# Performance work log

Measured on AMD Instinct MI355X. Metric: run time of the kernel, lower is better.

The kernel has to match this reference:

```python
import jax, jax.numpy as jnp
import numpy as np

N_NODES = 100000
N_EDGES = 1250000
D = 64


def _sage_conv(x, src, dst, W_l, b_l, W_r, n_nodes):
    # message = x[src]; scatter-mean onto dst; then lin_l(mean) + lin_r(x)
    msg = x[src]                                               # [E, D]
    agg = jax.ops.segment_sum(msg, dst, num_segments=n_nodes)  # [N, D]
    cnt = jax.ops.segment_sum(jnp.ones((src.shape[0],), x.dtype), dst,
                              num_segments=n_nodes)            # [N]
    mean = agg / jnp.maximum(cnt, 1.0)[:, None]
    return mean @ W_l + b_l + x @ W_r


def setup_inputs() -> dict:
    key = jax.random.key(0)
    ks = jax.random.split(key, 8)
    s = 1.0 / np.sqrt(D)
    x = jax.random.normal(ks[0], (N_NODES, D), dtype=jnp.float32)
    edge_index = jax.random.randint(ks[1], (2, N_EDGES), 0, N_NODES, dtype=jnp.int32)
    W_l1 = jax.random.normal(ks[2], (D, D), dtype=jnp.float32) * s
    b_l1 = jnp.zeros((D,), jnp.float32)
    W_r1 = jax.random.normal(ks[3], (D, D), dtype=jnp.float32) * s
    W_l2 = jax.random.normal(ks[4], (D, D), dtype=jnp.float32) * s
    b_l2 = jnp.zeros((D,), jnp.float32)
    W_r2 = jax.random.normal(ks[5], (D, D), dtype=jnp.float32) * s
    return {"x": x, "edge_index": edge_index,
            "W_l1": W_l1, "b_l1": b_l1, "W_r1": W_r1,
            "W_l2": W_l2, "b_l2": b_l2, "W_r2": W_r2}


def reference(x, edge_index, W_l1, b_l1, W_r1, W_l2, b_l2, W_r2):
    src, dst = edge_index[0], edge_index[1]
    n = x.shape[0]
    h = jax.nn.relu(_sage_conv(x, src, dst, W_l1, b_l1, W_r1, n))
    return _sage_conv(h, src, dst, W_l2, b_l2, W_r2, n)
```

## Files before the change

### kernel.cpp

```cpp
#include <hip/hip_runtime.h>

#define N_NODES 100000
#define N_EDGES 1250000
#define D 64

#define BIN_SHIFT 9
#define BIN_NODES 512
#define NBINS ((N_NODES + BIN_NODES - 1) >> BIN_SHIFT)
#define BIN_CAP 7168
#define SLAB 8704
#define CHUNK 4096
#define ZERO_NODE N_NODES

typedef __attribute__((ext_vector_type(8))) short short8;
typedef __attribute__((ext_vector_type(4))) float f32x4;

__device__ inline unsigned short f2bf(float f) {
    unsigned int u = __float_as_uint(f);
    unsigned int r = (u + 0x7fffu + ((u >> 16) & 1u)) >> 16;
    return (unsigned short)r;
}
__device__ inline float4 unpack_bf4(uint2 u) {
    float4 f;
    f.x = __uint_as_float(u.x << 16);
    f.y = __uint_as_float(u.x & 0xffff0000u);
    f.z = __uint_as_float(u.y << 16);
    f.w = __uint_as_float(u.y & 0xffff0000u);
    return f;
}

__global__ __launch_bounds__(256)
void convert_zero_kernel(const float4* __restrict__ xin, ushort4* __restrict__ xb,
                         int n4, int* __restrict__ bin_cnt,
                         unsigned int* __restrict__ xb_zrow,
                         unsigned int* __restrict__ h_zrow,
                         const float* __restrict__ Wl1, const float* __restrict__ Wr1,
                         const float* __restrict__ Wl2, const float* __restrict__ Wr2,
                         unsigned short* __restrict__ wt) {
    int i = blockIdx.x * 256 + threadIdx.x;
    if (i < n4) {
        float4 v = xin[i];
        ushort4 u;
        u.x = f2bf(v.x); u.y = f2bf(v.y); u.z = f2bf(v.z); u.w = f2bf(v.w);
        xb[i] = u;
    }
    if (i < NBINS) bin_cnt[i] = 0;
    if (i < 32) { xb_zrow[i] = 0u; h_zrow[i] = 0u; }
    if (i < 2 * 64 * 128) {
        int layer = i >> 13;
        int n = (i >> 7) & 63;
        int k = i & 127;
        const float* W = layer ? (k < 64 ? Wl2 : Wr2) : (k < 64 ? Wl1 : Wr1);
        float v = W[(k & 63) * D + n];
        wt[i] = f2bf(v);
    }
}

__global__ __launch_bounds__(256)
void bin_kernel(const int* __restrict__ src, const int* __restrict__ dst,
                int* __restrict__ bin_cnt, int* __restrict__ slabs) {
    __shared__ int lhist[NBINS];
    __shared__ int lstart[NBINS];
    __shared__ int lbase[NBINS];
    __shared__ int lcur[NBINS];
    __shared__ int pscan[256];
    __shared__ int sval[CHUNK];
    __shared__ int sdst[CHUNK];

    const int t = threadIdx.x;
    const int e0 = blockIdx.x * CHUNK;
    int cnt = N_EDGES - e0; if (cnt > CHUNK) cnt = CHUNK;

    for (int i = t; i < NBINS; i += 256) lhist[i] = 0;
    __syncthreads();

    for (int i = t; i < cnt; i += 256)
        atomicAdd(&lhist[dst[e0 + i] >> BIN_SHIFT], 1);
    __syncthreads();

    int h = (t < NBINS) ? lhist[t] : 0;
    pscan[t] = h;
    __syncthreads();
    for (int off = 1; off < 256; off <<= 1) {
        int x = (t >= off) ? pscan[t - off] : 0;
        __syncthreads();
        pscan[t] += x;
        __syncthreads();
    }
    if (t < NBINS) {
        int excl = pscan[t] - h;
        lstart[t] = excl;
        lcur[t] = excl;
        lbase[t] = (h > 0) ? atomicAdd(&bin_cnt[t], h) : 0;
    }
    __syncthreads();

    for (int i = t; i < cnt; i += 256) {
        int d = dst[e0 + i];
        int s = src[e0 + i];
        int b = d >> BIN_SHIFT;
        int slot = atomicAdd(&lcur[b], 1);
        int rank = slot - lstart[b];
        sval[slot] = (s << BIN_SHIFT) | (d & (BIN_NODES - 1));
        int gp = lbase[b] + rank;
        sdst[slot] = (gp < BIN_CAP) ? (b * SLAB + gp) : -1;
    }
    __syncthreads();

    for (int i = t; i < cnt; i += 256) {
        int dd = sdst[i];
        if (dd >= 0) slabs[dd] = sval[i];
    }
}

__global__ __launch_bounds__(256)
void bin_sort_kernel(int* __restrict__ slabs, const int* __restrict__ bin_cnt,
                     int* __restrict__ deg_out, int* __restrict__ rstart_out) {
    __shared__ int hist[BIN_NODES];
    __shared__ int cur[BIN_NODES];
    __shared__ int pscan[256];
    __shared__ int stage[BIN_CAP];

    const int b = blockIdx.x;
    const int t = threadIdx.x;
    int cnt = bin_cnt[b]; if (cnt > BIN_CAP) cnt = BIN_CAP;
    const int nb0 = b << BIN_SHIFT;
    const int nn = (N_NODES - nb0 < BIN_NODES) ? (N_NODES - nb0) : BIN_NODES;
    const int slab0 = b * SLAB;

    hist[t] = 0; hist[t + 256] = 0;
    __syncthreads();

    for (int i = t; i < cnt; i += 256) {
        int p = slabs[slab0 + i];
        stage[i] = p;
        atomicAdd(&hist[p & (BIN_NODES - 1)], 1);
    }
    __syncthreads();

    int h0 = hist[2 * t], h1 = hist[2 * t + 1];
    int ph0 = (h0 + 3) & ~3, ph1 = (h1 + 3) & ~3;
    int pv = ph0 + ph1;
    pscan[t] = pv;
    __syncthreads();
    for (int off = 1; off < 256; off <<= 1) {
        int x = (t >= off) ? pscan[t - off] : 0;
        __syncthreads();
        pscan[t] += x;
        __syncthreads();
    }
    int pairExcl = pscan[t] - pv;
    int s0 = pairExcl, s1 = pairExcl + ph0;
    cur[2 * t] = s0;
    cur[2 * t + 1] = s1;
    if (2 * t < nn) {
        deg_out[nb0 + 2 * t] = h0;
        rstart_out[nb0 + 2 * t] = slab0 + s0;
        for (int i = h0; i < ph0; ++i) slabs[slab0 + s0 + i] = ZERO_NODE;
    }
    if (2 * t + 1 < nn) {
        deg_out[nb0 + 2 * t + 1] = h1;
        rstart_out[nb0 + 2 * t + 1] = slab0 + s1;
        for (int i = h1; i < ph1; ++i) slabs[slab0 + s1 + i] = ZERO_NODE;
    }
    __syncthreads();

    for (int i = t; i < cnt; i += 256) {
        int p = stage[i];
        int pos = atomicAdd(&cur[p & (BIN_NODES - 1)], 1);
        slabs[slab0 + pos] = p >> BIN_SHIFT;
    }
}

template <typename TOUT>
__global__ __launch_bounds__(256, 8)
void fused_layer_kernel(const unsigned short* __restrict__ xin,
                        const int* __restrict__ rstart,
                        const int* __restrict__ deg,
                        const int* __restrict__ sorted_src,
                        const unsigned short* __restrict__ wt,
                        const float* __restrict__ bl,
                        TOUT* __restrict__ out,
                        int relu) {
    __shared__ __align__(16) unsigned short sA[32][136];

    const uint2* __restrict__ xin64 = (const uint2*)xin;

    const int tid = threadIdx.x;
    const int row0 = blockIdx.x * 32;

    const int wave = tid >> 6;
    const int lane = tid & 63;
    const int q  = lane >> 4;
    const int f2 = lane & 15;

    for (int r = wave; r < 32; r += 4) {
        int n = row0 + r;
        float4 a = make_float4(0.f, 0.f, 0.f, 0.f);
        int dg = deg[n];
        int pdg = (dg + 3) & ~3;
        int st = rstart[n];
        uint2 xraw = xin64[(size_t)n * 16 + f2];

        for (int base = 0; base < pdg; base += 64) {
            int m = pdg - base; if (m > 64) m = 64;
            int idx = 0;
            if (lane < m) idx = sorted_src[st + base + lane];
            int quads = m >> 2;
            float4 c0 = make_float4(0.f, 0.f, 0.f, 0.f);
            float4 c1 = make_float4(0.f, 0.f, 0.f, 0.f);
            float4 c2 = make_float4(0.f, 0.f, 0.f, 0.f);
            float4 c3 = make_float4(0.f, 0.f, 0.f, 0.f);
            int t = 0;
            for (; t + 4 <= quads; t += 4) {
                int sA_ = __shfl(idx, 4 * t + q);
                int sB_ = __shfl(idx, 4 * t + 4 + q);
                int sC_ = __shfl(idx, 4 * t + 8 + q);
                int sD_ = __shfl(idx, 4 * t + 12 + q);
                float4 fA = unpack_bf4(xin64[(size_t)sA_ * 16 + f2]);
                float4 fB = unpack_bf4(xin64[(size_t)sB_ * 16 + f2]);
                float4 fC = unpack_bf4(xin64[(size_t)sC_ * 16 + f2]);
                float4 fD = unpack_bf4(xin64[(size_t)sD_ * 16 + f2]);
                c0.x += fA.x; c0.y += fA.y; c0.z += fA.z; c0.w += fA.w;
                c1.x += fB.x; c1.y += fB.y; c1.z += fB.z; c1.w += fB.w;
                c2.x += fC.x; c2.y += fC.y; c2.z += fC.z; c2.w += fC.w;
                c3.x += fD.x; c3.y += fD.y; c3.z += fD.z; c3.w += fD.w;
            }
            for (; t + 2 <= quads; t += 2) {
                int sA_ = __shfl(idx, 4 * t + q);
                int sB_ = __shfl(idx, 4 * t + 4 + q);
                float4 fA = unpack_bf4(xin64[(size_t)sA_ * 16 + f2]);
                float4 fB = unpack_bf4(xin64[(size_t)sB_ * 16 + f2]);
                c0.x += fA.x; c0.y += fA.y; c0.z += fA.z; c0.w += fA.w;
                c1.x += fB.x; c1.y += fB.y; c1.z += fB.z; c1.w += fB.w;
            }
            for (; t < quads; ++t) {
                int sA_ = __shfl(idx, 4 * t + q);
                float4 fA = unpack_bf4(xin64[(size_t)sA_ * 16 + f2]);
                c0.x += fA.x; c0.y += fA.y; c0.z += fA.z; c0.w += fA.w;
            }
            a.x += (c0.x + c1.x) + (c2.x + c3.x);
            a.y += (c0.y + c1.y) + (c2.y + c3.y);
            a.z += (c0.z + c1.z) + (c2.z + c3.z);
            a.w += (c0.w + c1.w) + (c2.w + c3.w);
        }

        a.x += __shfl_xor(a.x, 16); a.y += __shfl_xor(a.y, 16);
        a.z += __shfl_xor(a.z, 16); a.w += __shfl_xor(a.w, 16);
        a.x += __shfl_xor(a.x, 32); a.y += __shfl_xor(a.y, 32);
        a.z += __shfl_xor(a.z, 32); a.w += __shfl_xor(a.w, 32);

        float inv = 1.0f / (float)(dg > 0 ? dg : 1);
        if (q == 0) {
            unsigned int p0 = (unsigned int)f2bf(a.x * inv) |
                              ((unsigned int)f2bf(a.y * inv) << 16);
            unsigned int p1 = (unsigned int)f2bf(a.z * inv) |
                              ((unsigned int)f2bf(a.w * inv) << 16);
            *(uint2*)&sA[r][f2 * 4] = make_uint2(p0, p1);
            *(uint2*)&sA[r][64 + f2 * 4] = xraw;
        }
    }
    __syncthreads();

    const int tm = wave & 1;
    const int tn0 = (wave >> 1) * 2;
    const int mrow = tm * 16 + (lane & 15);
    const int kq = (lane >> 4) * 8;

    short8 afr[4];
#pragma unroll
    for (int kk = 0; kk < 4; ++kk)
        afr[kk] = *(const short8*)&sA[mrow][kk * 32 + kq];

#pragma unroll
    for (int ti = 0; ti < 2; ++ti) {
        const int tn = tn0 + ti;
        const int col = tn * 16 + (lane & 15);
        float bias = bl[col];
        f32x4 acc = {bias, bias, bias, bias};
#pragma unroll
        for (int kk = 0; kk < 4; ++kk) {
            short8 bfr = *(const short8*)&wt[col * 128 + kk * 32 + kq];
            acc = __builtin_amdgcn_mfma_f32_16x16x32_bf16(afr[kk], bfr, acc, 0, 0, 0);
        }
        const int r0 = row0 + tm * 16 + (lane >> 4) * 4;
#pragma unroll
        for (int reg = 0; reg < 4; ++reg) {
            float o = relu ? fmaxf(acc[reg], 0.f) : acc[reg];
            if constexpr (__hip_internal::is_same<TOUT, unsigned short>::value)
                out[(size_t)(r0 + reg) * D + col] = f2bf(o);
            else
                out[(size_t)(r0 + reg) * D + col] = o;
        }
    }
}

extern "C" void kernel_launch(void* const* d_in, const int* in_sizes, int n_in,
                              void* d_out, int out_size, void* d_ws, size_t ws_size,
                              hipStream_t stream) {
    const float* x   = (const float*)d_in[0];
    const int*   ei  = (const int*)d_in[1];
    const float* Wl1 = (const float*)d_in[2];
    const float* b1  = (const float*)d_in[3];
    const float* Wr1 = (const float*)d_in[4];
    const float* Wl2 = (const float*)d_in[5];
    const float* b2  = (const float*)d_in[6];
    const float* Wr2 = (const float*)d_in[7];

    const int* src = ei;
    const int* dst = ei + N_EDGES;

    int* slabs   = (int*)d_ws;
    int* bin_cnt = slabs + (size_t)NBINS * SLAB;
    int* deg     = bin_cnt + 256;
    int* rstart  = deg + N_NODES;
    unsigned short* wt_all = (unsigned short*)(rstart + N_NODES);
    unsigned short* wt1 = wt_all;
    unsigned short* wt2 = wt_all + 64 * 128;
    unsigned short* h = wt_all + 2 * 64 * 128;
    float* out = (float*)d_out;
    unsigned short* xb = (unsigned short*)d_out;

    const int dense_blocks = N_NODES / 32;
    const int conv4 = N_NODES * D / 4;
    const int bin_blocks = (N_EDGES + CHUNK - 1) / CHUNK;

    convert_zero_kernel<<<(conv4 + 255) / 256, 256, 0, stream>>>(
        (const float4*)x, (ushort4*)xb, conv4, bin_cnt,
        (unsigned int*)(xb + (size_t)ZERO_NODE * D),
        (unsigned int*)(h + (size_t)ZERO_NODE * D),
        Wl1, Wr1, Wl2, Wr2, wt_all);

    bin_kernel<<<bin_blocks, 256, 0, stream>>>(src, dst, bin_cnt, slabs);
    bin_sort_kernel<<<NBINS, 256, 0, stream>>>(slabs, bin_cnt, deg, rstart);

    fused_layer_kernel<unsigned short><<<dense_blocks, 256, 0, stream>>>(
        xb, rstart, deg, slabs, wt1, b1, h, 1);
    fused_layer_kernel<float><<<dense_blocks, 256, 0, stream>>>(
        h, rstart, deg, slabs, wt2, b2, out, 0);
}
```

Baseline: 220.7 us.

## Halve bin size to 256 nodes and gather two rows per wave

Halves the destination bin size to 256 nodes, which gives about 391 bins and so twice as many bin-sort blocks. The local histogram scan now covers two bins per thread, and the sort kernel now scans in place in the cur array. The fused layer kernel processes two destination rows per wave at once, interleaving their neighbor gathers to expose more memory-level parallelism. The costs are extra register pressure, a smaller per-bin capacity (4096) that makes overflow more likely, and a larger bin_cnt region in the workspace.

```diff
diff --git a/kernel.cpp b/kernel.cpp
--- a/kernel.cpp
+++ b/kernel.cpp
@@ -4,12 +4,12 @@
 #define N_EDGES 1250000
 #define D 64
 
-#define BIN_SHIFT 9
-#define BIN_NODES 512
+#define BIN_SHIFT 8
+#define BIN_NODES 256
 #define NBINS ((N_NODES + BIN_NODES - 1) >> BIN_SHIFT)
-#define BIN_CAP 7168
-#define SLAB 8704
-#define CHUNK 4096
+#define BIN_CAP 4096
+#define SLAB (BIN_CAP + 3 * BIN_NODES)
+#define CHUNK 2048
 #define ZERO_NODE N_NODES
 
 typedef __attribute__((ext_vector_type(8))) short short8;
@@ -78,8 +78,10 @@
         atomicAdd(&lhist[dst[e0 + i] >> BIN_SHIFT], 1);
     __syncthreads();
 
-    int h = (t < NBINS) ? lhist[t] : 0;
-    pscan[t] = h;
+    int h0 = (2 * t < NBINS) ? lhist[2 * t] : 0;
+    int h1 = (2 * t + 1 < NBINS) ? lhist[2 * t + 1] : 0;
+    int pv = h0 + h1;
+    pscan[t] = pv;
     __syncthreads();
     for (int off = 1; off < 256; off <<= 1) {
         int x = (t >= off) ? pscan[t - off] : 0;
@@ -87,11 +89,14 @@
         pscan[t] += x;
         __syncthreads();
     }
-    if (t < NBINS) {
-        int excl = pscan[t] - h;
-        lstart[t] = excl;
-        lcur[t] = excl;
-        lbase[t] = (h > 0) ? atomicAdd(&bin_cnt[t], h) : 0;
+    int excl = pscan[t] - pv;
+    if (2 * t < NBINS) {
+        lstart[2 * t] = excl; lcur[2 * t] = excl;
+        lbase[2 * t] = (h0 > 0) ? atomicAdd(&bin_cnt[2 * t], h0) : 0;
+    }
+    if (2 * t + 1 < NBINS) {
+        lstart[2 * t + 1] = excl + h0; lcur[2 * t + 1] = excl + h0;
+        lbase[2 * t + 1] = (h1 > 0) ? atomicAdd(&bin_cnt[2 * t + 1], h1) : 0;
     }
     __syncthreads();
 
@@ -118,7 +123,6 @@
                      int* __restrict__ deg_out, int* __restrict__ rstart_out) {
     __shared__ int hist[BIN_NODES];
     __shared__ int cur[BIN_NODES];
-    __shared__ int pscan[256];
     __shared__ int stage[BIN_CAP];
 
     const int b = blockIdx.x;
@@ -128,7 +132,7 @@
     const int nn = (N_NODES - nb0 < BIN_NODES) ? (N_NODES - nb0) : BIN_NODES;
     const int slab0 = b * SLAB;
 
-    hist[t] = 0; hist[t + 256] = 0;
+    hist[t] = 0;
     __syncthreads();
 
     for (int i = t; i < cnt; i += 256) {
@@ -138,30 +142,24 @@
     }
     __syncthreads();
 
-    int h0 = hist[2 * t], h1 = hist[2 * t + 1];
-    int ph0 = (h0 + 3) & ~3, ph1 = (h1 + 3) & ~3;
-    int pv = ph0 + ph1;
-    pscan[t] = pv;
+    int h = hist[t];
+    int ph = (h + 3) & ~3;
+    int pv = ph;
+    cur[t] = pv;
     __syncthreads();
     for (int off = 1; off < 256; off <<= 1) {
-        int x = (t >= off) ? pscan[t - off] : 0;
+        int x = (t >= off) ? cur[t - off] : 0;
         __syncthreads();
-        pscan[t] += x;
+        cur[t] += x;
         __syncthreads();
     }
-    int pairExcl = pscan[t] - pv;
-    int s0 = pairExcl, s1 = pairExcl + ph0;
-    cur[2 * t] = s0;
-    cur[2 * t + 1] = s1;
-    if (2 * t < nn) {
-        deg_out[nb0 + 2 * t] = h0;
-        rstart_out[nb0 + 2 * t] = slab0 + s0;
-        for (int i = h0; i < ph0; ++i) slabs[slab0 + s0 + i] = ZERO_NODE;
-    }
-    if (2 * t + 1 < nn) {
-        deg_out[nb0 + 2 * t + 1] = h1;
-        rstart_out[nb0 + 2 * t + 1] = slab0 + s1;
-        for (int i = h1; i < ph1; ++i) slabs[slab0 + s1 + i] = ZERO_NODE;
+    int excl = cur[t] - pv;
+    __syncthreads();
+    cur[t] = excl;
+    if (t < nn) {
+        deg_out[nb0 + t] = h;
+        rstart_out[nb0 + t] = slab0 + excl;
+        for (int i = h; i < ph; ++i) slabs[slab0 + excl + i] = ZERO_NODE;
     }
     __syncthreads();
 
@@ -170,6 +168,47 @@
         int pos = atomicAdd(&cur[p & (BIN_NODES - 1)], 1);
         slabs[slab0 + pos] = p >> BIN_SHIFT;
     }
+}
+
+__device__ inline void gather_batch(const uint2* __restrict__ xin64, int idx,
+                                    int m, int q, int f2, float4& a) {
+    int quads = m >> 2;
+    float4 c0 = make_float4(0.f, 0.f, 0.f, 0.f);
+    float4 c1 = make_float4(0.f, 0.f, 0.f, 0.f);
+    float4 c2 = make_float4(0.f, 0.f, 0.f, 0.f);
+    float4 c3 = make_float4(0.f, 0.f, 0.f, 0.f);
+    int t = 0;
+    for (; t + 4 <= quads; t += 4) {
+        int sA = __shfl(idx, 4 * t + q);
+        int sB = __shfl(idx, 4 * t + 4 + q);
+        int sC = __shfl(idx, 4 * t + 8 + q);
+        int sD = __shfl(idx, 4 * t + 12 + q);
+        float4 fA = unpack_bf4(xin64[(size_t)sA * 16 + f2]);
+        float4 fB = unpack_bf4(xin64[(size_t)sB * 16 + f2]);
+        float4 fC = unpack_bf4(xin64[(size_t)sC * 16 + f2]);
+        float4 fD = unpack_bf4(xin64[(size_t)sD * 16 + f2]);
+        c0.x += fA.x; c0.y += fA.y; c0.z += fA.z; c0.w += fA.w;
+        c1.x += fB.x; c1.y += fB.y; c1.z += fB.z; c1.w += fB.w;
+        c2.x += fC.x; c2.y += fC.y; c2.z += fC.z; c2.w += fC.w;
+        c3.x += fD.x; c3.y += fD.y; c3.z += fD.z; c3.w += fD.w;
+    }
+    for (; t + 2 <= quads; t += 2) {
+        int sA = __shfl(idx, 4 * t + q);
+        int sB = __shfl(idx, 4 * t + 4 + q);
+        float4 fA = unpack_bf4(xin64[(size_t)sA * 16 + f2]);
+        float4 fB = unpack_bf4(xin64[(size_t)sB * 16 + f2]);
+        c0.x += fA.x; c0.y += fA.y; c0.z += fA.z; c0.w += fA.w;
+        c1.x += fB.x; c1.y += fB.y; c1.z += fB.z; c1.w += fB.w;
+    }
+    for (; t < quads; ++t) {
+        int sA = __shfl(idx, 4 * t + q);
+        float4 fA = unpack_bf4(xin64[(size_t)sA * 16 + f2]);
+        c0.x += fA.x; c0.y += fA.y; c0.z += fA.z; c0.w += fA.w;
+    }
+    a.x += (c0.x + c1.x) + (c2.x + c3.x);
+    a.y += (c0.y + c1.y) + (c2.y + c3.y);
+    a.z += (c0.z + c1.z) + (c2.z + c3.z);
+    a.w += (c0.w + c1.w) + (c2.w + c3.w);
 }
 
 template <typename TOUT>
@@ -194,70 +233,51 @@
     const int q  = lane >> 4;
     const int f2 = lane & 15;
 
-    for (int r = wave; r < 32; r += 4) {
-        int n = row0 + r;
-        float4 a = make_float4(0.f, 0.f, 0.f, 0.f);
-        int dg = deg[n];
-        int pdg = (dg + 3) & ~3;
-        int st = rstart[n];
-        uint2 xraw = xin64[(size_t)n * 16 + f2];
-
-        for (int base = 0; base < pdg; base += 64) {
-            int m = pdg - base; if (m > 64) m = 64;
-            int idx = 0;
-            if (lane < m) idx = sorted_src[st + base + lane];
-            int quads = m >> 2;
-            float4 c0 = make_float4(0.f, 0.f, 0.f, 0.f);
-            float4 c1 = make_float4(0.f, 0.f, 0.f, 0.f);
-            float4 c2 = make_float4(0.f, 0.f, 0.f, 0.f);
-            float4 c3 = make_float4(0.f, 0.f, 0.f, 0.f);
-            int t = 0;
-            for (; t + 4 <= quads; t += 4) {
-                int sA_ = __shfl(idx, 4 * t + q);
-                int sB_ = __shfl(idx, 4 * t + 4 + q);
-                int sC_ = __shfl(idx, 4 * t + 8 + q);
-                int sD_ = __shfl(idx, 4 * t + 12 + q);
-                float4 fA = unpack_bf4(xin64[(size_t)sA_ * 16 + f2]);
-                float4 fB = unpack_bf4(xin64[(size_t)sB_ * 16 + f2]);
-                float4 fC = unpack_bf4(xin64[(size_t)sC_ * 16 + f2]);
-                float4 fD = unpack_bf4(xin64[(size_t)sD_ * 16 + f2]);
-                c0.x += fA.x; c0.y += fA.y; c0.z += fA.z; c0.w += fA.w;
-                c1.x += fB.x; c1.y += fB.y; c1.z += fB.z; c1.w += fB.w;
-                c2.x += fC.x; c2.y += fC.y; c2.z += fC.z; c2.w += fC.w;
-                c3.x += fD.x; c3.y += fD.y; c3.z += fD.z; c3.w += fD.w;
-            }
-            for (; t + 2 <= quads; t += 2) {
-                int sA_ = __shfl(idx, 4 * t + q);
-                int sB_ = __shfl(idx, 4 * t + 4 + q);
-                float4 fA = unpack_bf4(xin64[(size_t)sA_ * 16 + f2]);
-                float4 fB = unpack_bf4(xin64[(size_t)sB_ * 16 + f2]);
-                c0.x += fA.x; c0.y += fA.y; c0.z += fA.z; c0.w += fA.w;
-                c1.x += fB.x; c1.y += fB.y; c1.z += fB.z; c1.w += fB.w;
-            }
-            for (; t < quads; ++t) {
-                int sA_ = __shfl(idx, 4 * t + q);
-                float4 fA = unpack_bf4(xin64[(size_t)sA_ * 16 + f2]);
-                c0.x += fA.x; c0.y += fA.y; c0.z += fA.z; c0.w += fA.w;
-            }
-            a.x += (c0.x + c1.x) + (c2.x + c3.x);
-            a.y += (c0.y + c1.y) + (c2.y + c3.y);
-            a.z += (c0.z + c1.z) + (c2.z + c3.z);
-            a.w += (c0.w + c1.w) + (c2.w + c3.w);
+    for (int r = wave; r < 32; r += 8) {
+        int n1 = row0 + r;
+        int n2 = row0 + r + 4;
+        int dg1 = deg[n1], dg2 = deg[n2];
+        int pdg1 = (dg1 + 3) & ~3, pdg2 = (dg2 + 3) & ~3;
+        int st1 = rstart[n1], st2 = rstart[n2];
+        uint2 xraw1 = xin64[(size_t)n1 * 16 + f2];
+        uint2 xraw2 = xin64[(size_t)n2 * 16 + f2];
+        float4 a1 = make_float4(0.f, 0.f, 0.f, 0.f);
+        float4 a2 = make_float4(0.f, 0.f, 0.f, 0.f);
+
+        for (int base = 0; base < pdg1 || base < pdg2; base += 64) {
+            int m1 = pdg1 - base; if (m1 > 64) m1 = 64;
+            int m2 = pdg2 - base; if (m2 > 64) m2 = 64;
+            int idx1 = 0, idx2 = 0;
+            if (lane < m1) idx1 = sorted_src[st1 + base + lane];
+            if (lane < m2) idx2 = sorted_src[st2 + base + lane];
+            if (m1 > 0) gather_batch(xin64, idx1, m1, q, f2, a1);
+            if (m2 > 0) gather_batch(xin64, idx2, m2, q, f2, a2);
         }
 
-        a.x += __shfl_xor(a.x, 16); a.y += __shfl_xor(a.y, 16);
-        a.z += __shfl_xor(a.z, 16); a.w += __shfl_xor(a.w, 16);
-        a.x += __shfl_xor(a.x, 32); a.y += __shfl_xor(a.y, 32);
-        a.z += __shfl_xor(a.z, 32); a.w += __shfl_xor(a.w, 32);
-
-        float inv = 1.0f / (float)(dg > 0 ? dg : 1);
+        a1.x += __shfl_xor(a1.x, 16); a1.y += __shfl_xor(a1.y, 16);
+        a1.z += __shfl_xor(a1.z, 16); a1.w += __shfl_xor(a1.w, 16);
+        a1.x += __shfl_xor(a1.x, 32); a1.y += __shfl_xor(a1.y, 32);
+        a1.z += __shfl_xor(a1.z, 32); a1.w += __shfl_xor(a1.w, 32);
+        a2.x += __shfl_xor(a2.x, 16); a2.y += __shfl_xor(a2.y, 16);
+        a2.z += __shfl_xor(a2.z, 16); a2.w += __shfl_xor(a2.w, 16);
+        a2.x += __shfl_xor(a2.x, 32); a2.y += __shfl_xor(a2.y, 32);
+        a2.z += __shfl_xor(a2.z, 32); a2.w += __shfl_xor(a2.w, 32);
+
         if (q == 0) {
-            unsigned int p0 = (unsigned int)f2bf(a.x * inv) |
-                              ((unsigned int)f2bf(a.y * inv) << 16);
-            unsigned int p1 = (unsigned int)f2bf(a.z * inv) |
-                              ((unsigned int)f2bf(a.w * inv) << 16);
+            float inv1 = 1.0f / (float)(dg1 > 0 ? dg1 : 1);
+            float inv2 = 1.0f / (float)(dg2 > 0 ? dg2 : 1);
+            unsigned int p0 = (unsigned int)f2bf(a1.x * inv1) |
+                              ((unsigned int)f2bf(a1.y * inv1) << 16);
+            unsigned int p1 = (unsigned int)f2bf(a1.z * inv1) |
+                              ((unsigned int)f2bf(a1.w * inv1) << 16);
             *(uint2*)&sA[r][f2 * 4] = make_uint2(p0, p1);
-            *(uint2*)&sA[r][64 + f2 * 4] = xraw;
+            *(uint2*)&sA[r][64 + f2 * 4] = xraw1;
+            p0 = (unsigned int)f2bf(a2.x * inv2) |
+                 ((unsigned int)f2bf(a2.y * inv2) << 16);
+            p1 = (unsigned int)f2bf(a2.z * inv2) |
+                 ((unsigned int)f2bf(a2.w * inv2) << 16);
+            *(uint2*)&sA[r + 4][f2 * 4] = make_uint2(p0, p1);
+            *(uint2*)&sA[r + 4][64 + f2 * 4] = xraw2;
         }
     }
     __syncthreads();
@@ -312,7 +332,7 @@
 
     int* slabs   = (int*)d_ws;
     int* bin_cnt = slabs + (size_t)NBINS * SLAB;
-    int* deg     = bin_cnt + 256;
+    int* deg     = bin_cnt + 512;
     int* rstart  = deg + N_NODES;
     unsigned short* wt_all = (unsigned short*)(rstart + N_NODES);
     unsigned short* wt1 = wt_all;
```

New measurement: 250.9 us. 13.7% more time.
